# Performance work log

Hardware: AMD Instinct MI355X
Metric: run time of the kernel (lower is better)

## Reference

```python
import jax, jax.numpy as jnp
import numpy as np

B, S, D = 2, 2048, 1024
H, DH = 16, 64  # n_heads, d_head = d_model // n_heads


def setup_inputs() -> dict:
    key = jax.random.key(0)
    ks = jax.random.split(key, 12)
    scale = 1.0 / np.sqrt(D)
    return {
        "queries": jax.random.normal(ks[0], (B, S, D), jnp.float32),
        "keys": jax.random.normal(ks[1], (B, S, D), jnp.float32),
        "values": jax.random.normal(ks[2], (B, S, D), jnp.float32),
        "mask": jax.random.randint(ks[3], (1, 1, S, S), 0, 2, jnp.int32),
        "Wq": jax.random.normal(ks[4], (D, D), jnp.float32) * scale,
        "bq": jnp.zeros((D,), jnp.float32),
        "Wk": jax.random.normal(ks[5], (D, D), jnp.float32) * scale,
        "bk": jnp.zeros((D,), jnp.float32),
        "Wv": jax.random.normal(ks[6], (D, D), jnp.float32) * scale,
        "bv": jnp.zeros((D,), jnp.float32),
        "Wo": jax.random.normal(ks[7], (D, D), jnp.float32) * scale,
        "bo": jnp.zeros((D,), jnp.float32),
    }


def _split_proj(x):
    # (B, ?, H, DH) reshape then permute -> (B, H, ?, DH)
    b = x.shape[0]
    return x.reshape(b, -1, H, DH).transpose(0, 2, 1, 3)


def reference(queries, keys, values, mask, Wq, bq, Wk, bk, Wv, bv, Wo, bo):
    q = queries @ Wq.T + bq
    k = keys @ Wk.T + bk
    v = values @ Wv.T + bv
    # NOTE: original source applies split_proj to queries twice (faithful repro)
    q = _split_proj(_split_proj(q))
    k = _split_proj(k)
    v = _split_proj(v)
    scores = jnp.einsum('bhqd,bhkd->bhqk', q, k) / jnp.sqrt(jnp.float32(DH))
    scores = scores + mask.astype(scores.dtype) * (-1e9)
    attn = jax.nn.softmax(scores, axis=-1)
    out = jnp.einsum('bhqk,bhkd->bhqd', attn, v)  # (B,H,S,DH)
    out = out.transpose(0, 2, 1, 3).reshape(out.shape[0], -1, D)
    return out @ Wo.T + bo
```

## Files before the change

### kernel.cpp

```cpp
#include <hip/hip_runtime.h>
#include <hip/hip_bf16.h>
#include <cstddef>
#include <cstdint>


typedef __attribute__((ext_vector_type(8))) short bf16x8;
typedef __attribute__((ext_vector_type(4))) float f32x4;

__device__ __forceinline__ void gl_lds16(const void* g, void* l) {
    __builtin_amdgcn_global_load_lds(
        (const __attribute__((address_space(1))) void*)g,
        (__attribute__((address_space(3))) void*)l, 16, 0, 0);
}

__global__ __launch_bounds__(256) void convert_all(
    const float* __restrict__ q, const float* __restrict__ k, const float* __restrict__ v,
    const float* __restrict__ wq, const float* __restrict__ wk,
    const float* __restrict__ wv, const float* __restrict__ wo,
    __hip_bfloat16* __restrict__ dq, __hip_bfloat16* __restrict__ dk,
    __hip_bfloat16* __restrict__ dv, __hip_bfloat16* __restrict__ dwq,
    __hip_bfloat16* __restrict__ dwk, __hip_bfloat16* __restrict__ dwv,
    __hip_bfloat16* __restrict__ dwo)
{
    const int bid = blockIdx.x;
    const float* s; __hip_bfloat16* d; int base;
    if      (bid < 2048) { s = q;  d = dq;  base = bid; }
    else if (bid < 4096) { s = k;  d = dk;  base = bid - 2048; }
    else if (bid < 6144) { s = v;  d = dv;  base = bid - 4096; }
    else if (bid < 6656) { s = wq; d = dwq; base = bid - 6144; }
    else if (bid < 7168) { s = wk; d = dwk; base = bid - 6656; }
    else if (bid < 7680) { s = wv; d = dwv; base = bid - 7168; }
    else                 { s = wo; d = dwo; base = bid - 7680; }
    const size_t i = (size_t)base * 256 + threadIdx.x;
    const float4* sp = (const float4*)s + i * 2;
    float4 v0 = sp[0], v1 = sp[1];
    union { __hip_bfloat16 h[8]; int4 qd; } u;
    u.h[0] = __float2bfloat16(v0.x); u.h[1] = __float2bfloat16(v0.y);
    u.h[2] = __float2bfloat16(v0.z); u.h[3] = __float2bfloat16(v0.w);
    u.h[4] = __float2bfloat16(v1.x); u.h[5] = __float2bfloat16(v1.y);
    u.h[6] = __float2bfloat16(v1.z); u.h[7] = __float2bfloat16(v1.w);
    *((int4*)d + i) = u.qd;
}

__global__ __launch_bounds__(256) void packmask(const int* __restrict__ mask,
                                                unsigned long long* __restrict__ mbits)
{
    const int wid  = (blockIdx.x * 256 + threadIdx.x) >> 6;
    const int lane = threadIdx.x & 63;
    const int qr = wid >> 5, w64 = wid & 31;
    const int m = mask[(size_t)qr * 2048 + w64 * 64 + lane];
    const unsigned long long bal = __ballot(m != 0);
    if (lane == 0) mbits[(size_t)qr * 32 + w64] = bal;
}

template <typename OutT>
__device__ __forceinline__ void gemm_body(
    const __hip_bfloat16* __restrict__ A, const __hip_bfloat16* __restrict__ Bm,
    const float* __restrict__ bias, OutT* __restrict__ C,
    int N, int m0, int n0, int brow,
    __hip_bfloat16* As, __hip_bfloat16* Bs)
{
    const int t = threadIdx.x, lane = t & 63, w = t >> 6;
    const int l15 = lane & 15, g = lane >> 4;
    const int wr = w >> 1, wc = w & 1;

    f32x4 acc[4][4] = {};

    for (int k0 = 0; k0 < 1024; k0 += 64) {
        __syncthreads();
        #pragma unroll
        for (int it = 0; it < 4; ++it) {
            const int chunk = it * 256 + w * 64 + lane;
            const int row = chunk >> 3, c = chunk & 7;
            gl_lds16(A  + (size_t)(m0 + row) * 1024 + k0 + c * 8, (char*)As + chunk * 16);
            gl_lds16(Bm + (size_t)(n0 + row) * 1024 + k0 + c * 8, (char*)Bs + chunk * 16);
        }
        __syncthreads();
        #pragma unroll
        for (int kk = 0; kk < 64; kk += 32) {
            bf16x8 af[4], bfr[4];
            #pragma unroll
            for (int i = 0; i < 4; ++i)
                af[i] = *(const bf16x8*)((const char*)As + (wr * 64 + i * 16 + l15) * 128 + kk * 2 + g * 16);
            #pragma unroll
            for (int j = 0; j < 4; ++j)
                bfr[j] = *(const bf16x8*)((const char*)Bs + (wc * 64 + j * 16 + l15) * 128 + kk * 2 + g * 16);
            #pragma unroll
            for (int i = 0; i < 4; ++i)
                #pragma unroll
                for (int j = 0; j < 4; ++j)
                    acc[i][j] = __builtin_amdgcn_mfma_f32_16x16x32_bf16(af[i], bfr[j], acc[i][j], 0, 0, 0);
        }
    }

    #pragma unroll
    for (int i = 0; i < 4; ++i) {
        const int m = m0 + wr * 64 + i * 16 + g * 4;
        #pragma unroll
        for (int j = 0; j < 4; ++j) {
            const int n = n0 + wc * 64 + j * 16 + l15;
            const float bc = brow ? 0.f : bias[n];
            #pragma unroll
            for (int r = 0; r < 4; ++r) {
                const float v = acc[i][j][r] + (brow ? bias[m + r] : bc);
                C[(size_t)(m + r) * N + n] = (OutT)v;
            }
        }
    }
}

__global__ __launch_bounds__(256) void qkv_gemm(
    const __hip_bfloat16* __restrict__ qin, const __hip_bfloat16* __restrict__ kin,
    const __hip_bfloat16* __restrict__ vin,
    const __hip_bfloat16* __restrict__ Wqb, const __hip_bfloat16* __restrict__ Wkb,
    const __hip_bfloat16* __restrict__ Wvb,
    const float* __restrict__ bq, const float* __restrict__ bk, const float* __restrict__ bv,
    __hip_bfloat16* __restrict__ qbuf, __hip_bfloat16* __restrict__ kbuf,
    __hip_bfloat16* __restrict__ vtb)
{
    __shared__ __align__(16) __hip_bfloat16 As[128 * 64];
    __shared__ __align__(16) __hip_bfloat16 Bs[128 * 64];
    const int z = blockIdx.z;
    if (z == 0)
        gemm_body(qin, Wqb, bq, qbuf, 1024, blockIdx.y * 128, blockIdx.x * 128, 0, As, Bs);
    else if (z == 1)
        gemm_body(kin, Wkb, bk, kbuf, 1024, blockIdx.y * 128, blockIdx.x * 128, 0, As, Bs);
    else
        gemm_body(Wvb, vin, bv, vtb, 4096, blockIdx.x * 128, blockIdx.y * 128, 1, As, Bs);
}

__global__ __launch_bounds__(256) void out_gemm(
    const __hip_bfloat16* __restrict__ A, const __hip_bfloat16* __restrict__ Bm,
    const float* __restrict__ bias, float* __restrict__ C)
{
    __shared__ __align__(16) __hip_bfloat16 As[128 * 64];
    __shared__ __align__(16) __hip_bfloat16 Bs[128 * 64];
    gemm_body(A, Bm, bias, C, 1024, blockIdx.y * 128, blockIdx.x * 128, 0, As, Bs);
}

__global__ __launch_bounds__(512) void attn_mfma(
    const __hip_bfloat16* __restrict__ qb,
    const __hip_bfloat16* __restrict__ kb,
    const __hip_bfloat16* __restrict__ vt,
    const unsigned long long* __restrict__ mbits,
    __hip_bfloat16* __restrict__ ctx)
{
    __shared__ __align__(16) __hip_bfloat16 Qs[128 * 64];
    __shared__ __align__(16) __hip_bfloat16 Ks[2][64 * 64];
    __shared__ __align__(16) __hip_bfloat16 Vs[2][64 * 64];
    __shared__ __align__(16) __hip_bfloat16 Pb[8][16 * 64];

    const int t = threadIdx.x, lane = t & 63, w = t >> 6;
    const int l15 = lane & 15, g = lane >> 4;
    const int q0 = blockIdx.x * 128;
    const int bh = blockIdx.y, b = bh >> 4, a = bh & 15;
    const int hq = blockIdx.x;

    constexpr float SC_LOG2E = 0.18033688011112042f;
    constexpr float OFFC     = -17.312340490667561f;
    constexpr float MASKB    = -1.0e9f;

    #pragma unroll
    for (int it = 0; it < 2; ++it) {
        const int c = it * 512 + t;
        const int row = c >> 3, cc = c & 7;
        const int cs = cc ^ (row & 7);
        const int s = row * 16 + a;
        gl_lds16(qb + (size_t)(b * 2048 + s) * 1024 + hq * 64 + cs * 8,
                 (char*)Qs + c * 16);
    }

    auto stage_kv = [&](int buf, int kt) {
        const int c = t;
        const int row = c >> 3, cc = c & 7;
        const int cs = cc ^ (row & 7);
        gl_lds16(kb + (size_t)(b * 2048 + kt * 64 + row) * 1024 + a * 64 + cs * 8,
                 (char*)Ks + buf * 8192 + c * 16);
        gl_lds16(vt + (size_t)(a * 64 + row) * 4096 + b * 2048 + kt * 64 + cs * 8,
                 (char*)Vs + buf * 8192 + c * 16);
    };

    stage_kv(0, 0);
    __syncthreads();

    f32x4 accd[4] = {};
    float l_r = 0.f;
    const int qrow = w * 16 + l15;
    const int qg = q0 + qrow;

    for (int kt = 0; kt < 32; ++kt) {
        const int cur = kt & 1;
        if (kt < 31) stage_kv(cur ^ 1, kt + 1);

        const uint2 mw = *(const uint2*)&mbits[(size_t)qg * 32 + kt];

        f32x4 sf[4] = {};
        #pragma unroll
        for (int half = 0; half < 2; ++half) {
            const int kc = half * 4 + g;
            const bf16x8 qf = *(const bf16x8*)((const char*)Qs + qrow * 128 + ((kc ^ (qrow & 7)) << 4));
            #pragma unroll
            for (int nf = 0; nf < 4; ++nf) {
                const int krow = nf * 16 + l15;
                const bf16x8 kf = *(const bf16x8*)((const char*)Ks + cur * 8192 + krow * 128 + ((kc ^ (krow & 7)) << 4));
                sf[nf] = __builtin_amdgcn_mfma_f32_16x16x32_bf16(kf, qf, sf[nf], 0, 0, 0);
            }
        }

        float psum = 0.f;
        #pragma unroll
        for (int nf = 0; nf < 4; ++nf) {
            const unsigned word = (nf & 2) ? mw.y : mw.x;
            const int bsh = ((nf & 1) << 4) + (g << 2);
            float pr[4];
            #pragma unroll
            for (int r = 0; r < 4; ++r) {
                const bool msk = (word >> (bsh + r)) & 1u;
                pr[r] = exp2f(fmaf(sf[nf][r], SC_LOG2E, msk ? MASKB : OFFC));
            }
            psum += (pr[0] + pr[1]) + (pr[2] + pr[3]);
            __hip_bfloat16 h0 = __float2bfloat16(pr[0]), h1 = __float2bfloat16(pr[1]);
            __hip_bfloat16 h2 = __float2bfloat16(pr[2]), h3 = __float2bfloat16(pr[3]);
            const unsigned w0 = (unsigned)*(unsigned short*)&h0 | ((unsigned)*(unsigned short*)&h1 << 16);
            const unsigned w1 = (unsigned)*(unsigned short*)&h2 | ((unsigned)*(unsigned short*)&h3 << 16);
            char* pb = (char*)Pb + w * 2048 + l15 * 128 +
                       (((2 * nf + (g >> 1)) ^ (l15 & 7)) << 4) + ((g & 1) << 3);
            *(uint2*)pb = make_uint2(w0, w1);
        }
        psum += __shfl_xor(psum, 16);
        psum += __shfl_xor(psum, 32);
        l_r += psum;

        #pragma unroll
        for (int jj = 0; jj < 2; ++jj) {
            const bf16x8 pa = *(const bf16x8*)((const char*)Pb + w * 2048 + l15 * 128 +
                                               (((4 * jj + g) ^ (l15 & 7)) << 4));
            #pragma unroll
            for (int df = 0; df < 4; ++df) {
                const int vrow = df * 16 + l15;
                const bf16x8 vf = *(const bf16x8*)((const char*)Vs + cur * 8192 + vrow * 128 +
                                                   (((4 * jj + g) ^ (vrow & 7)) << 4));
                accd[df] = __builtin_amdgcn_mfma_f32_16x16x32_bf16(pa, vf, accd[df], 0, 0, 0);
            }
        }

        __syncthreads();
    }

    #pragma unroll
    for (int r = 0; r < 4; ++r) {
        const float lq = __shfl(l_r, (g << 2) + r);
        const float inv = 1.0f / lq;
        const int q = q0 + w * 16 + (g << 2) + r;
        #pragma unroll
        for (int df = 0; df < 4; ++df)
            ctx[(size_t)(b * 2048 + q) * 1024 + (a << 6) + df * 16 + l15] =
                __float2bfloat16(accd[df][r] * inv);
    }
}

extern "C" void kernel_launch(void* const* d_in, const int* in_sizes, int n_in,
                              void* d_out, int out_size, void* d_ws, size_t ws_size,
                              hipStream_t stream)
{
    const float* queries = (const float*)d_in[0];
    const float* keys    = (const float*)d_in[1];
    const float* values  = (const float*)d_in[2];
    const int*   mask    = (const int*)  d_in[3];
    const float* Wq = (const float*)d_in[4];
    const float* bq = (const float*)d_in[5];
    const float* Wk = (const float*)d_in[6];
    const float* bk = (const float*)d_in[7];
    const float* Wv = (const float*)d_in[8];
    const float* bv = (const float*)d_in[9];
    const float* Wo = (const float*)d_in[10];
    const float* bo = (const float*)d_in[11];

    const size_t NM = (size_t)4096 * 1024;
    const size_t NW = (size_t)1024 * 1024;
    __hip_bfloat16* p = (__hip_bfloat16*)d_ws;
    __hip_bfloat16* qin = p;  p += NM;
    __hip_bfloat16* kin = p;  p += NM;
    __hip_bfloat16* vin = p;  p += NM;
    __hip_bfloat16* Wqb = p;  p += NW;
    __hip_bfloat16* Wkb = p;  p += NW;
    __hip_bfloat16* Wvb = p;  p += NW;
    __hip_bfloat16* Wob = p;  p += NW;
    __hip_bfloat16* qbuf = p; p += NM;
    __hip_bfloat16* kbuf = p; p += NM;
    __hip_bfloat16* vtb  = p; p += NM;
    unsigned long long* mbits = (unsigned long long*)p;
    __hip_bfloat16* ctxb = qin;

    convert_all<<<dim3(8192), dim3(256), 0, stream>>>(
        queries, keys, values, Wq, Wk, Wv, Wo,
        qin, kin, vin, Wqb, Wkb, Wvb, Wob);
    packmask<<<dim3(16384), dim3(256), 0, stream>>>(mask, mbits);

    qkv_gemm<<<dim3(8, 32, 3), dim3(256), 0, stream>>>(
        qin, kin, vin, Wqb, Wkb, Wvb, bq, bk, bv, qbuf, kbuf, vtb);

    attn_mfma<<<dim3(16, 32), dim3(512), 0, stream>>>(qbuf, kbuf, vtb, mbits, ctxb);

    out_gemm<<<dim3(8, 32), dim3(256), 0, stream>>>(ctxb, Wob, bo, (float*)d_out);
}
```

Before: 178.8 us.

## Shrink attention blocks to 64 queries with XCD-aware mapping and register Q

The attention kernel now launches 1024 blocks of 256 threads, each covering 64 query rows instead of 128, with a block index remapping that groups heads by XCD for L2 locality. Q fragments are held in registers rather than LDS, and K/V double-buffering is replaced by a single buffer loaded between two barriers, with launch bounds set for 6 blocks per CU. The aim is more blocks in flight and less LDS per block, which should hide latency through occupancy. The cost is that K/V loads are no longer overlapped with compute inside a block, and each K/V tile is fetched twice as often across blocks.

Measured after the change: 190.5 us. 6.5% more time.

```diff
diff --git a/kernel.cpp b/kernel.cpp
--- a/kernel.cpp
+++ b/kernel.cpp
@@ -138,72 +138,66 @@
     gemm_body(A, Bm, bias, C, 1024, blockIdx.y * 128, blockIdx.x * 128, 0, As, Bs);
 }
 
-__global__ __launch_bounds__(512) void attn_mfma(
+__global__ __launch_bounds__(256, 6) void attn_mfma(
     const __hip_bfloat16* __restrict__ qb,
     const __hip_bfloat16* __restrict__ kb,
     const __hip_bfloat16* __restrict__ vt,
     const unsigned long long* __restrict__ mbits,
     __hip_bfloat16* __restrict__ ctx)
 {
-    __shared__ __align__(16) __hip_bfloat16 Qs[128 * 64];
-    __shared__ __align__(16) __hip_bfloat16 Ks[2][64 * 64];
-    __shared__ __align__(16) __hip_bfloat16 Vs[2][64 * 64];
-    __shared__ __align__(16) __hip_bfloat16 Pb[8][16 * 64];
+    __shared__ __align__(16) __hip_bfloat16 Ks[64 * 64];
+    __shared__ __align__(16) __hip_bfloat16 Vs[64 * 64];
+    __shared__ __align__(16) __hip_bfloat16 Pb[4][16 * 64];
 
     const int t = threadIdx.x, lane = t & 63, w = t >> 6;
     const int l15 = lane & 15, g = lane >> 4;
-    const int q0 = blockIdx.x * 128;
-    const int bh = blockIdx.y, b = bh >> 4, a = bh & 15;
-    const int hq = blockIdx.x;
+
+    const int bid = blockIdx.x;
+    const int xcd = bid & 7, i = bid >> 3;
+    const int bh = xcd * 4 + (i >> 5), qt = i & 31;
+    const int b = bh >> 4, a = bh & 15;
+    const int q0 = qt * 64;
+    const int hq = q0 >> 7;
 
     constexpr float SC_LOG2E = 0.18033688011112042f;
     constexpr float OFFC     = -17.312340490667561f;
     constexpr float MASKB    = -1.0e9f;
 
+    const int qrow = w * 16 + l15;
+    const int s = ((q0 & 64) + qrow) * 16 + a;
+    bf16x8 qreg[2];
     #pragma unroll
-    for (int it = 0; it < 2; ++it) {
-        const int c = it * 512 + t;
-        const int row = c >> 3, cc = c & 7;
-        const int cs = cc ^ (row & 7);
-        const int s = row * 16 + a;
-        gl_lds16(qb + (size_t)(b * 2048 + s) * 1024 + hq * 64 + cs * 8,
-                 (char*)Qs + c * 16);
-    }
-
-    auto stage_kv = [&](int buf, int kt) {
-        const int c = t;
-        const int row = c >> 3, cc = c & 7;
-        const int cs = cc ^ (row & 7);
-        gl_lds16(kb + (size_t)(b * 2048 + kt * 64 + row) * 1024 + a * 64 + cs * 8,
-                 (char*)Ks + buf * 8192 + c * 16);
-        gl_lds16(vt + (size_t)(a * 64 + row) * 4096 + b * 2048 + kt * 64 + cs * 8,
-                 (char*)Vs + buf * 8192 + c * 16);
-    };
-
-    stage_kv(0, 0);
-    __syncthreads();
+    for (int half = 0; half < 2; ++half)
+        qreg[half] = *(const bf16x8*)&qb[(size_t)(b * 2048 + s) * 1024 + hq * 64 + (half * 4 + g) * 8];
 
     f32x4 accd[4] = {};
     float l_r = 0.f;
-    const int qrow = w * 16 + l15;
     const int qg = q0 + qrow;
 
     for (int kt = 0; kt < 32; ++kt) {
-        const int cur = kt & 1;
-        if (kt < 31) stage_kv(cur ^ 1, kt + 1);
-
+        __syncthreads();
+        #pragma unroll
+        for (int it = 0; it < 2; ++it) {
+            const int c = it * 256 + t;
+            const int row = c >> 3, cc = c & 7;
+            const int cs = cc ^ (row & 7);
+            gl_lds16(kb + (size_t)(b * 2048 + kt * 64 + row) * 1024 + a * 64 + cs * 8,
+                     (char*)Ks + c * 16);
+            gl_lds16(vt + (size_t)(a * 64 + row) * 4096 + b * 2048 + kt * 64 + cs * 8,
+                     (char*)Vs + c * 16);
+        }
         const uint2 mw = *(const uint2*)&mbits[(size_t)qg * 32 + kt];
+        __syncthreads();
 
         f32x4 sf[4] = {};
         #pragma unroll
         for (int half = 0; half < 2; ++half) {
             const int kc = half * 4 + g;
-            const bf16x8 qf = *(const bf16x8*)((const char*)Qs + qrow * 128 + ((kc ^ (qrow & 7)) << 4));
             #pragma unroll
             for (int nf = 0; nf < 4; ++nf) {
                 const int krow = nf * 16 + l15;
-                const bf16x8 kf = *(const bf16x8*)((const char*)Ks + cur * 8192 + krow * 128 + ((kc ^ (krow & 7)) << 4));
-                sf[nf] = __builtin_amdgcn_mfma_f32_16x16x32_bf16(kf, qf, sf[nf], 0, 0, 0);
+                const bf16x8 kf = *(const bf16x8*)((const char*)Ks + krow * 128 + ((kc ^ (krow & 7)) << 4));
+                sf[nf] = __builtin_amdgcn_mfma_f32_16x16x32_bf16(kf, qreg[half], sf[nf], 0, 0, 0);
             }
         }
 
@@ -238,13 +232,11 @@
             #pragma unroll
             for (int df = 0; df < 4; ++df) {
                 const int vrow = df * 16 + l15;
-                const bf16x8 vf = *(const bf16x8*)((const char*)Vs + cur * 8192 + vrow * 128 +
+                const bf16x8 vf = *(const bf16x8*)((const char*)Vs + vrow * 128 +
                                                    (((4 * jj + g) ^ (vrow & 7)) << 4));
                 accd[df] = __builtin_amdgcn_mfma_f32_16x16x32_bf16(pa, vf, accd[df], 0, 0, 0);
             }
         }
-
-        __syncthreads();
     }
 
     #pragma unroll
@@ -300,7 +292,7 @@
     qkv_gemm<<<dim3(8, 32, 3), dim3(256), 0, stream>>>(
         qin, kin, vin, Wqb, Wkb, Wvb, bq, bk, bv, qbuf, kbuf, vtb);
 
-    attn_mfma<<<dim3(16, 32), dim3(512), 0, stream>>>(qbuf, kbuf, vtb, mbits, ctxb);
+    attn_mfma<<<dim3(1024), dim3(256), 0, stream>>>(qbuf, kbuf, vtb, mbits, ctxb);
 
     out_gemm<<<dim3(8, 32), dim3(256), 0, stream>>>(ctxb, Wob, bo, (float*)d_out);
 }
```
